# Kernel optimization log

Measured on AMD Instinct MI355X. Metric: run time of the kernel, lower is better.

Reference implementation:

```python
import jax, jax.numpy as jnp
import numpy as np

BLOCK = 8

def _make_dct_consts(block=BLOCK):
    idx = np.arange(block)
    c = np.cos((2 * idx[:, None] + 1) * idx[None, :] * np.pi / (2 * block)).astype(np.float32)  # [x, u]
    dct = c[:, None, :, None] * c[None, :, None, :]  # [x, y, u, v]
    alpha = np.ones(block, dtype=np.float32)
    alpha[0] = 1.0 / np.sqrt(2.0)
    scale = (np.outer(alpha, alpha) * 0.25).astype(np.float32)  # [u, v]
    return jnp.asarray(dct), jnp.asarray(scale)


def setup_inputs() -> dict:
    key = jax.random.key(0)
    x = jax.random.uniform(key, (262144, 3, BLOCK, BLOCK), dtype=jnp.float32) * 255.0
    dct_tensor, scale = _make_dct_consts()
    return {"x": x, "dct_tensor": dct_tensor, "scale": scale}


def reference(x, dct_tensor, scale):
    # o = x - 128; out[b,c,u,v] = scale[u,v] * sum_{x,y} o[b,c,x,y] * T[x,y,u,v]
    o = x - 128.0
    out = jnp.einsum("bcxy,xyuv->bcuv", o, dct_tensor)
    return scale * out
```

## Files before the change

### kernel.cpp

```cpp
#include <hip/hip_runtime.h>


typedef float vfloat4 __attribute__((ext_vector_type(4)));

__device__ __forceinline__ float uniformf(float v)
{
    return __int_as_float(__builtin_amdgcn_readfirstlane(__float_as_int(v)));
}

__device__ __forceinline__ void xpose8(float a[8], bool h1, bool h2, bool h4)
{
#pragma unroll
    for (int j = 0; j < 8; j += 2) {
        const int k = j + 1;
        float fj = __shfl_xor(a[k], 1);
        float fk = __shfl_xor(a[j], 1);
        float nj = h1 ? fj : a[j];
        float nk = h1 ? a[k] : fk;
        a[j] = nj; a[k] = nk;
    }
#pragma unroll
    for (int jj = 0; jj < 8; jj += 4) {
#pragma unroll
        for (int j0 = 0; j0 < 2; ++j0) {
            const int j = jj + j0, k = j + 2;
            float fj = __shfl_xor(a[k], 2);
            float fk = __shfl_xor(a[j], 2);
            float nj = h2 ? fj : a[j];
            float nk = h2 ? a[k] : fk;
            a[j] = nj; a[k] = nk;
        }
    }
#pragma unroll
    for (int j = 0; j < 4; ++j) {
        const int k = j + 4;
        float fj = __shfl_xor(a[k], 4);
        float fk = __shfl_xor(a[j], 4);
        float nj = h4 ? fj : a[j];
        float nk = h4 ? a[k] : fk;
        a[j] = nj; a[k] = nk;
    }
}

__device__ __forceinline__ void dct_block(const float o[8], float res[8],
                                          const float cs[8][8],
                                          bool h1, bool h2, bool h4)
{
    float t[8];
#pragma unroll
    for (int u = 0; u < 8; ++u) {
        float s = 0.0f;
#pragma unroll
        for (int xx = 0; xx < 8; ++xx) s = fmaf(o[xx], cs[xx][u], s);
        t[u] = s;
    }
    xpose8(t, h1, h2, h4);
#pragma unroll
    for (int v = 0; v < 8; ++v) {
        float s = 0.0f;
#pragma unroll
        for (int y = 0; y < 8; ++y) s = fmaf(t[y], cs[y][v], s);
        res[v] = s;
    }
}

__global__ __launch_bounds__(256) void dct2d_kernel(
    const float* __restrict__ x,
    const float* __restrict__ dct,
    const float* __restrict__ scale,
    float* __restrict__ out,
    int nblocks)
{
    const int tid  = blockIdx.x * blockDim.x + threadIdx.x;
    const int lane = tid & 7;
    const int g    = tid >> 3;
    const int ngroups = (gridDim.x * blockDim.x) >> 3;

    float cs[8][8];
#pragma unroll
    for (int b = 0; b < 8; ++b) {
        const float a05 = scale[b * 8] * 2.8284271247461903f;
#pragma unroll
        for (int a = 0; a < 8; ++a)
            cs[a][b] = uniformf(dct[a * 512 + b * 8] * a05);
    }

    const bool h1 = (lane & 1) != 0;
    const bool h2 = (lane & 2) != 0;
    const bool h4 = (lane & 4) != 0;

    int b0 = 2 * g;
    for (; b0 + 1 < nblocks; b0 += 2 * ngroups) {
        const float* p = x + (size_t)b0 * 64 + lane;
        float oA[8], oB[8];
#pragma unroll
        for (int xx = 0; xx < 8; ++xx) oA[xx] = p[xx * 8];
#pragma unroll
        for (int xx = 0; xx < 8; ++xx) oB[xx] = p[64 + xx * 8];
#pragma unroll
        for (int xx = 0; xx < 8; ++xx) { oA[xx] -= 128.0f; oB[xx] -= 128.0f; }

        float rA[8], rB[8];
        dct_block(oA, rA, cs, h1, h2, h4);
        dct_block(oB, rB, cs, h1, h2, h4);

        float* op = out + (size_t)b0 * 64 + lane * 8;
        vfloat4 sA0 = { rA[0], rA[1], rA[2], rA[3] };
        vfloat4 sA1 = { rA[4], rA[5], rA[6], rA[7] };
        vfloat4 sB0 = { rB[0], rB[1], rB[2], rB[3] };
        vfloat4 sB1 = { rB[4], rB[5], rB[6], rB[7] };
        __builtin_nontemporal_store(sA0, reinterpret_cast<vfloat4*>(op));
        __builtin_nontemporal_store(sA1, reinterpret_cast<vfloat4*>(op + 4));
        __builtin_nontemporal_store(sB0, reinterpret_cast<vfloat4*>(op + 64));
        __builtin_nontemporal_store(sB1, reinterpret_cast<vfloat4*>(op + 68));
    }
    if (b0 < nblocks) {
        const float* p = x + (size_t)b0 * 64 + lane;
        float o[8];
#pragma unroll
        for (int xx = 0; xx < 8; ++xx) o[xx] = p[xx * 8] - 128.0f;
        float r[8];
        dct_block(o, r, cs, h1, h2, h4);
        float* op = out + (size_t)b0 * 64 + lane * 8;
        vfloat4 s0 = { r[0], r[1], r[2], r[3] };
        vfloat4 s1 = { r[4], r[5], r[6], r[7] };
        __builtin_nontemporal_store(s0, reinterpret_cast<vfloat4*>(op));
        __builtin_nontemporal_store(s1, reinterpret_cast<vfloat4*>(op + 4));
    }
}

extern "C" void kernel_launch(void* const* d_in, const int* in_sizes, int n_in,
                              void* d_out, int out_size, void* d_ws, size_t ws_size,
                              hipStream_t stream)
{
    const float* x     = (const float*)d_in[0];
    const float* dct   = (const float*)d_in[1];
    const float* scale = (const float*)d_in[2];
    float* out = (float*)d_out;

    int nblocks = in_sizes[0] / 64;
    int block = 256;
    int grid  = 2048;

    dct2d_kernel<<<grid, block, 0, stream>>>(x, dct, scale, out, nblocks);
}
```

Measured before the change: 76.75 us.

## Stage input tiles through per-wave LDS with coalesced vec4 loads

Each wave now loads a 16-block tile with coalesced 16-byte vector loads and writes it into a swizzled per-wave LDS buffer. Threads then read their column data from LDS instead of issuing strided scalar global loads. The goal is fewer, wider global memory transactions on a bandwidth-bound kernel. In exchange it adds LDS traffic and 16KB of shared memory per block, which may lower occupancy. No barrier is used because each wave only touches its own LDS slot.

```diff
diff --git a/kernel.cpp b/kernel.cpp
--- a/kernel.cpp
+++ b/kernel.cpp
@@ -71,10 +71,18 @@
     float* __restrict__ out,
     int nblocks)
 {
-    const int tid  = blockIdx.x * blockDim.x + threadIdx.x;
-    const int lane = tid & 7;
-    const int g    = tid >> 3;
-    const int ngroups = (gridDim.x * blockDim.x) >> 3;
+    __shared__ float lds_all[4][1024];
+
+    const int tid   = blockIdx.x * blockDim.x + threadIdx.x;
+    const int lane  = threadIdx.x & 63;
+    const int wslot = threadIdx.x >> 6;
+    const int gwid  = tid >> 6;
+    const int nwaves = (gridDim.x * blockDim.x) >> 6;
+    const int g    = lane >> 3;
+    const int r    = lane & 7;
+    const int kg   = g & 3;
+
+    float* L = lds_all[wslot];
 
     float cs[8][8];
 #pragma unroll
@@ -85,26 +93,41 @@
             cs[a][b] = uniformf(dct[a * 512 + b * 8] * a05);
     }
 
-    const bool h1 = (lane & 1) != 0;
-    const bool h2 = (lane & 2) != 0;
-    const bool h4 = (lane & 4) != 0;
+    const bool h1 = (r & 1) != 0;
+    const bool h2 = (r & 2) != 0;
+    const bool h4 = (r & 4) != 0;
 
-    int b0 = 2 * g;
-    for (; b0 + 1 < nblocks; b0 += 2 * ngroups) {
-        const float* p = x + (size_t)b0 * 64 + lane;
+    int wws[4];
+#pragma unroll
+    for (int i = 0; i < 4; ++i) {
+        int Wt = i * 256 + lane * 4;
+        wws[i] = Wt ^ (((Wt >> 7) & 3) << 3);
+    }
+    int aoff[8];
+#pragma unroll
+    for (int xx = 0; xx < 8; ++xx) aoff[xx] = 128 * g + 8 * (xx ^ kg) + r;
+
+    const int ntiles = nblocks >> 4;
+    for (int tile = gwid; tile < ntiles; tile += nwaves) {
+        const vfloat4* src = reinterpret_cast<const vfloat4*>(x + (size_t)tile * 1024);
+        vfloat4 v0 = src[lane];
+        vfloat4 v1 = src[64 + lane];
+        vfloat4 v2 = src[128 + lane];
+        vfloat4 v3 = src[192 + lane];
+        *reinterpret_cast<vfloat4*>(&L[wws[0]]) = v0;
+        *reinterpret_cast<vfloat4*>(&L[wws[1]]) = v1;
+        *reinterpret_cast<vfloat4*>(&L[wws[2]]) = v2;
+        *reinterpret_cast<vfloat4*>(&L[wws[3]]) = v3;
         float oA[8], oB[8];
 #pragma unroll
-        for (int xx = 0; xx < 8; ++xx) oA[xx] = p[xx * 8];
-#pragma unroll
-        for (int xx = 0; xx < 8; ++xx) oB[xx] = p[64 + xx * 8];
-#pragma unroll
-        for (int xx = 0; xx < 8; ++xx) { oA[xx] -= 128.0f; oB[xx] -= 128.0f; }
-
+        for (int xx = 0; xx < 8; ++xx) {
+            oA[xx] = L[aoff[xx]]      - 128.0f;
+            oB[xx] = L[aoff[xx] + 64] - 128.0f;
+        }
         float rA[8], rB[8];
         dct_block(oA, rA, cs, h1, h2, h4);
         dct_block(oB, rB, cs, h1, h2, h4);
-
-        float* op = out + (size_t)b0 * 64 + lane * 8;
+        float* op = out + (size_t)(tile * 16 + 2 * g) * 64 + r * 8;
         vfloat4 sA0 = { rA[0], rA[1], rA[2], rA[3] };
         vfloat4 sA1 = { rA[4], rA[5], rA[6], rA[7] };
         vfloat4 sB0 = { rB[0], rB[1], rB[2], rB[3] };
@@ -114,18 +137,27 @@
         __builtin_nontemporal_store(sB0, reinterpret_cast<vfloat4*>(op + 64));
         __builtin_nontemporal_store(sB1, reinterpret_cast<vfloat4*>(op + 68));
     }
-    if (b0 < nblocks) {
-        const float* p = x + (size_t)b0 * 64 + lane;
-        float o[8];
+
+    const int rem  = nblocks & 15;
+    if (rem && gwid == 0) {
+        const int base = ntiles * 16;
 #pragma unroll
-        for (int xx = 0; xx < 8; ++xx) o[xx] = p[xx * 8] - 128.0f;
-        float r[8];
-        dct_block(o, r, cs, h1, h2, h4);
-        float* op = out + (size_t)b0 * 64 + lane * 8;
-        vfloat4 s0 = { r[0], r[1], r[2], r[3] };
-        vfloat4 s1 = { r[4], r[5], r[6], r[7] };
-        __builtin_nontemporal_store(s0, reinterpret_cast<vfloat4*>(op));
-        __builtin_nontemporal_store(s1, reinterpret_cast<vfloat4*>(op + 4));
+        for (int pass = 0; pass < 2; ++pass) {
+            int bi = base + g + pass * 8;
+            if (bi < nblocks) {
+                const float* p = x + (size_t)bi * 64 + r;
+                float o[8];
+#pragma unroll
+                for (int xx = 0; xx < 8; ++xx) o[xx] = p[xx * 8] - 128.0f;
+                float rr[8];
+                dct_block(o, rr, cs, h1, h2, h4);
+                float* op = out + (size_t)bi * 64 + r * 8;
+                vfloat4 s0 = { rr[0], rr[1], rr[2], rr[3] };
+                vfloat4 s1 = { rr[4], rr[5], rr[6], rr[7] };
+                __builtin_nontemporal_store(s0, reinterpret_cast<vfloat4*>(op));
+                __builtin_nontemporal_store(s1, reinterpret_cast<vfloat4*>(op + 4));
+            }
+        }
     }
 }
 
```

New measurement: 84.18 us. 1.1x slower.
